# Kernel optimization log

Hardware: AMD Instinct MI355X
Metric: run time of the kernel (lower is better)

The kernel has to match this reference:

```python
import jax, jax.numpy as jnp
import numpy as np

MEM = 256
K = 4
SQRT_MK = 32  # sqrt(MEM*K)
HID = 1024
INP = 1024
B = 8192
EPS = 1e-12


def _linear_params(key, out_f, in_f):
    kw, kb = jax.random.split(key)
    bound = 1.0 / np.sqrt(in_f)
    W = jax.random.uniform(kw, (out_f, in_f), jnp.float32, -bound, bound)
    b = jax.random.uniform(kb, (out_f,), jnp.float32, -bound, bound)
    return W, b


def setup_inputs() -> dict:
    key = jax.random.key(0)
    ks = jax.random.split(key, 8)
    x = jax.random.normal(ks[0], (B, INP), jnp.float32)
    h0 = jax.random.normal(ks[1], (B, HID), jnp.float32)
    memory = jax.random.normal(ks[2], (B, MEM), jnp.float32)
    W_h, b_h = _linear_params(ks[3], HID, MEM + HID + INP)        # hmi2h
    W_a, b_a = _linear_params(ks[4], K, MEM + HID)                # hm2alpha
    W_b, b_b = _linear_params(ks[5], K, MEM + HID)                # hm2beta
    W_va, b_va = _linear_params(ks[6], 2 * SQRT_MK, MEM + HID)    # hm2v_alpha
    W_vb, b_vb = _linear_params(ks[7], 2 * SQRT_MK, MEM + HID)    # hm2v_beta
    return {"x": x, "h0": h0, "memory": memory,
            "W_h": W_h, "b_h": b_h, "W_a": W_a, "b_a": b_a,
            "W_b": W_b, "b_b": b_b, "W_va": W_va, "b_va": b_va,
            "W_vb": W_vb, "b_vb": b_vb}


def _p5_normalize(v):
    # F.normalize(p=5, dim=2): v / max(||v||_5, eps)
    n = jnp.sum(jnp.abs(v) ** 5, axis=2, keepdims=True) ** (1.0 / 5.0)
    return v / jnp.maximum(n, EPS)


def _rank1_v(hm, W, b):
    u = hm @ W.T + b                       # [B, 2*sqrt_mk]
    u0, u1 = u[:, :SQRT_MK], u[:, SQRT_MK:]
    v = (u0[:, :, None] * u1[:, None, :]).reshape(-1, K, MEM)  # outer product
    return _p5_normalize(v)


def reference(x, h0, memory, W_h, b_h, W_a, b_a, W_b, b_b, W_va, b_va, W_vb, b_vb):
    # use_relu=False -> _opt_relu is identity; layer_norm=False -> identity
    c_input = jnp.concatenate([x, h0, memory], axis=1)          # [B, INP+HID+MEM]
    h = jax.nn.relu(c_input @ W_h.T + b_h)                      # [B, HID]
    hm = jnp.concatenate([h, memory], axis=1)                   # [B, HID+MEM]
    alpha = hm @ W_a.T + b_a                                    # [B, K]
    beta = hm @ W_b.T + b_b                                     # [B, K]
    v_alpha = _rank1_v(hm, W_va, b_va)                          # [B, K, MEM]
    v_beta = _rank1_v(hm, W_vb, b_vb)                           # [B, K, MEM]
    delta = alpha[:, :, None] * v_alpha - beta[:, :, None] * v_beta
    memory_new = memory + jnp.mean(delta, axis=1)               # [B, MEM]
    return memory_new, h
```

## Files before the change

### kernel.cpp

```cpp
#include <hip/hip_runtime.h>
#include <stdint.h>

#define B_ROWS 8192
#define INP    1024
#define HID    1024
#define MEMD   256
#define KIN    2304
#define KHM    1280
#define NCAT   144

typedef unsigned short u16;
typedef unsigned int   u32;
typedef __attribute__((ext_vector_type(8))) short bf16x8;
typedef __attribute__((ext_vector_type(4))) float f32x4;

__device__ __forceinline__ u16 f2bf(float f) {
  u32 b = __builtin_bit_cast(u32, f);
  u32 r = b + 0x7FFF + ((b >> 16) & 1);
  return (u16)(r >> 16);
}

__device__ __forceinline__ void gload16(const void* g, void* l) {
  __builtin_amdgcn_global_load_lds(
      (const __attribute__((address_space(1))) u32*)g,
      (__attribute__((address_space(3))) u32*)l, 16, 0, 0);
}

__global__ void k_cvt_xh(const float* __restrict__ x, const float* __restrict__ h0,
                         u16* __restrict__ Abig) {
  const int nIter = B_ROWS * 2048 / 8;
  for (int i = blockIdx.x * blockDim.x + threadIdx.x; i < nIter;
       i += gridDim.x * blockDim.x) {
    int row = i >> 8;
    int col = (i & 255) * 8;
    const float* src = (col < 1024) ? (x + (size_t)row * 1024 + col)
                                    : (h0 + (size_t)row * 1024 + (col - 1024));
    float4 v0 = ((const float4*)src)[0];
    float4 v1 = ((const float4*)src)[1];
    union { u16 u[8]; uint4 q; } pk;
    pk.u[0]=f2bf(v0.x); pk.u[1]=f2bf(v0.y); pk.u[2]=f2bf(v0.z); pk.u[3]=f2bf(v0.w);
    pk.u[4]=f2bf(v1.x); pk.u[5]=f2bf(v1.y); pk.u[6]=f2bf(v1.z); pk.u[7]=f2bf(v1.w);
    *((uint4*)(Abig + (size_t)row * KIN + col)) = pk.q;
  }
}

__global__ void k_cvt_mem(const float* __restrict__ mem,
                          u16* __restrict__ Abig, u16* __restrict__ hm) {
  int i = blockIdx.x * blockDim.x + threadIdx.x;
  int row = i >> 5;
  int col = (i & 31) * 8;
  const float* src = mem + (size_t)row * MEMD + col;
  float4 v0 = ((const float4*)src)[0];
  float4 v1 = ((const float4*)src)[1];
  union { u16 u[8]; uint4 q; } pk;
  pk.u[0]=f2bf(v0.x); pk.u[1]=f2bf(v0.y); pk.u[2]=f2bf(v0.z); pk.u[3]=f2bf(v0.w);
  pk.u[4]=f2bf(v1.x); pk.u[5]=f2bf(v1.y); pk.u[6]=f2bf(v1.z); pk.u[7]=f2bf(v1.w);
  *((uint4*)(Abig + (size_t)row * KIN + 2048 + col)) = pk.q;
  *((uint4*)(hm   + (size_t)row * KHM + 1024 + col)) = pk.q;
}

__global__ void k_cvt_wh(const float* __restrict__ Wh, u16* __restrict__ WhB) {
  int i = blockIdx.x * blockDim.x + threadIdx.x;
  const float* src = Wh + (size_t)i * 8;
  float4 v0 = ((const float4*)src)[0];
  float4 v1 = ((const float4*)src)[1];
  union { u16 u[8]; uint4 q; } pk;
  pk.u[0]=f2bf(v0.x); pk.u[1]=f2bf(v0.y); pk.u[2]=f2bf(v0.z); pk.u[3]=f2bf(v0.w);
  pk.u[4]=f2bf(v1.x); pk.u[5]=f2bf(v1.y); pk.u[6]=f2bf(v1.z); pk.u[7]=f2bf(v1.w);
  *((uint4*)(WhB + (size_t)i * 8)) = pk.q;
}

__global__ void k_cvt_wcat(const float* __restrict__ Wa, const float* __restrict__ ba,
                           const float* __restrict__ Wb, const float* __restrict__ bb,
                           const float* __restrict__ Wva, const float* __restrict__ bva,
                           const float* __restrict__ Wvb, const float* __restrict__ bvb,
                           u16* __restrict__ Wcat, float* __restrict__ bcat) {
  int r = blockIdx.x;
  int t = threadIdx.x;
  const float* src = nullptr; float bias = 0.f;
  if      (r < 4)   { src = Wa  + (size_t)r        * KHM; bias = ba[r];      }
  else if (r < 8)   { src = Wb  + (size_t)(r - 4)  * KHM; bias = bb[r - 4];  }
  else if (r < 72)  { src = Wva + (size_t)(r - 8)  * KHM; bias = bva[r - 8]; }
  else if (r < 136) { src = Wvb + (size_t)(r - 72) * KHM; bias = bvb[r - 72];}
  if (t == 0) bcat[r] = bias;
  if (t < 160) {
    int col = t * 8;
    union { u16 u[8]; uint4 q; } pk;
    if (src) {
      float4 v0 = ((const float4*)(src + col))[0];
      float4 v1 = ((const float4*)(src + col))[1];
      pk.u[0]=f2bf(v0.x); pk.u[1]=f2bf(v0.y); pk.u[2]=f2bf(v0.z); pk.u[3]=f2bf(v0.w);
      pk.u[4]=f2bf(v1.x); pk.u[5]=f2bf(v1.y); pk.u[6]=f2bf(v1.z); pk.u[7]=f2bf(v1.w);
    } else {
      pk.q = make_uint4(0, 0, 0, 0);
    }
    *((uint4*)(Wcat + (size_t)r * KHM + col)) = pk.q;
  }
}

__global__ void __launch_bounds__(256, 2)
k_gemm1(const u16* __restrict__ Abig, const u16* __restrict__ WhB,
        const float* __restrict__ bh,
        float* __restrict__ outH, u16* __restrict__ hm) {
  __shared__ u16 As[2][128 * 64];
  __shared__ u16 Bs[2][128 * 64];
  const int tid = threadIdx.x;
  const int bid = blockIdx.x;
  const int swz = (bid & 7) * 64 + (bid >> 3);
  const int br = swz >> 3;
  const int bc = swz & 7;
  const int wid = tid >> 6, lane = tid & 63;
  const int wr = wid >> 1, wc = wid & 1;
  const int lr = lane & 15, lko = lane >> 4;

  const f32x4 vz = {0.f, 0.f, 0.f, 0.f};
  f32x4 acc[4][4];
#pragma unroll
  for (int m = 0; m < 4; ++m)
#pragma unroll
    for (int n = 0; n < 4; ++n) acc[m][n] = vz;

  const int sRow   = tid >> 3;
  const int sSlotG = (tid & 7) ^ (sRow & 7);
  const u16* gA = Abig + (size_t)(br * 128 + sRow) * KIN + sSlotG * 8;
  const u16* gB = WhB  + (size_t)(bc * 128 + sRow) * KIN + sSlotG * 8;

  const int sx  = lr & 7;
  const int s0  = ((0 + lko) ^ sx) * 8;
  const int s1  = ((4 + lko) ^ sx) * 8;
  const int axr = (wr * 64 + lr) * 64;
  const int bxr = (wc * 64 + lr) * 64;

#pragma unroll
  for (int q = 0; q < 4; ++q) {
    gload16(gA + (size_t)(q * 32) * KIN, &As[0][q * 2048 + tid * 8]);
    gload16(gB + (size_t)(q * 32) * KIN, &Bs[0][q * 2048 + tid * 8]);
  }

  for (int kt = 0; kt < KIN / 64; ++kt) {
    const int cur = kt & 1;
    if (kt < KIN / 64 - 1) {
      const int kofs = (kt + 1) * 64;
#pragma unroll
      for (int q = 0; q < 4; ++q) {
        gload16(gA + (size_t)(q * 32) * KIN + kofs, &As[1 - cur][q * 2048 + tid * 8]);
        gload16(gB + (size_t)(q * 32) * KIN + kofs, &Bs[1 - cur][q * 2048 + tid * 8]);
      }
      asm volatile("s_waitcnt vmcnt(8)" ::: "memory");
    } else {
      asm volatile("s_waitcnt vmcnt(0)" ::: "memory");
    }
    __builtin_amdgcn_s_barrier();
    __builtin_amdgcn_sched_barrier(0);

    const u16* Ac = &As[cur][0];
    const u16* Bc = &Bs[cur][0];
    {
      bf16x8 a[4], b[4];
#pragma unroll
      for (int m = 0; m < 4; ++m) a[m] = *(const bf16x8*)&Ac[axr + m * 1024 + s0];
#pragma unroll
      for (int n = 0; n < 4; ++n) b[n] = *(const bf16x8*)&Bc[bxr + n * 1024 + s0];
      __builtin_amdgcn_s_setprio(1);
#pragma unroll
      for (int m = 0; m < 4; ++m)
#pragma unroll
        for (int n = 0; n < 4; ++n)
          acc[m][n] = __builtin_amdgcn_mfma_f32_16x16x32_bf16(a[m], b[n], acc[m][n], 0, 0, 0);
      __builtin_amdgcn_s_setprio(0);
    }
    {
      bf16x8 a[4], b[4];
#pragma unroll
      for (int m = 0; m < 4; ++m) a[m] = *(const bf16x8*)&Ac[axr + m * 1024 + s1];
#pragma unroll
      for (int n = 0; n < 4; ++n) b[n] = *(const bf16x8*)&Bc[bxr + n * 1024 + s1];
      __builtin_amdgcn_s_setprio(1);
#pragma unroll
      for (int m = 0; m < 4; ++m)
#pragma unroll
        for (int n = 0; n < 4; ++n)
          acc[m][n] = __builtin_amdgcn_mfma_f32_16x16x32_bf16(a[m], b[n], acc[m][n], 0, 0, 0);
      __builtin_amdgcn_s_setprio(0);
    }
    __builtin_amdgcn_sched_barrier(0);
    __builtin_amdgcn_s_barrier();
  }

  const int rowBase = br * 128 + wr * 64;
  const int colBase = bc * 128 + wc * 64;
#pragma unroll
  for (int n = 0; n < 4; ++n) {
    const int col = colBase + n * 16 + lr;
    const float bias = bh[col];
#pragma unroll
    for (int m = 0; m < 4; ++m) {
#pragma unroll
      for (int r = 0; r < 4; ++r) {
        const int row = rowBase + m * 16 + lko * 4 + r;
        float v = fmaxf(acc[m][n][r] + bias, 0.0f);
        outH[(size_t)row * HID + col] = v;
        hm[(size_t)row * KHM + col] = f2bf(v);
      }
    }
  }
}

__device__ __forceinline__ float p5(float x) {
  float a = fabsf(x);
  float a2 = a * a;
  return a2 * a2 * a;
}

__global__ void __launch_bounds__(256, 2)
k_gemm2(const u16* __restrict__ hm, const u16* __restrict__ Wcat,
        const float* __restrict__ bcat,
        const float* __restrict__ mem, float* __restrict__ outM) {
  __shared__ float pS[4][16][148];
  const int tid = threadIdx.x;
  const int bid = blockIdx.x;
  const int wid = tid >> 6, lane = tid & 63;
  const int lr = lane & 15, lko = lane >> 4;
  const int rowBase = bid * 16;

  const f32x4 vz = {0.f, 0.f, 0.f, 0.f};
  f32x4 acc[9];
#pragma unroll
  for (int n = 0; n < 9; ++n) acc[n] = vz;

  const u16* gA = hm   + (size_t)(rowBase + lr) * KHM + lko * 8;
  const u16* gB = Wcat + (size_t)lr * KHM + lko * 8;

  for (int c = 0; c < 5; ++c) {
    const int kofs = (c * 4 + wid) * 64;
#pragma unroll
    for (int h = 0; h < 2; ++h) {
      const int ko = kofs + h * 32;
      bf16x8 a = *(const bf16x8*)(gA + ko);
      bf16x8 b[9];
#pragma unroll
      for (int n = 0; n < 9; ++n)
        b[n] = *(const bf16x8*)(gB + (size_t)(n * 16) * KHM + ko);
#pragma unroll
      for (int n = 0; n < 9; ++n)
        acc[n] = __builtin_amdgcn_mfma_f32_16x16x32_bf16(a, b[n], acc[n], 0, 0, 0);
    }
  }

#pragma unroll
  for (int n = 0; n < 9; ++n)
#pragma unroll
    for (int r = 0; r < 4; ++r)
      pS[wid][lko * 4 + r][n * 16 + lr] = acc[n][r];
  __syncthreads();

  {
    const int rr = tid >> 4;
    const int cb = (tid & 15) * 9;
#pragma unroll
    for (int i = 0; i < 9; ++i) {
      const int col = cb + i;
      float s = pS[0][rr][col] + pS[1][rr][col] + pS[2][rr][col] + pS[3][rr][col]
              + bcat[col];
      pS[0][rr][col] = s;
    }
  }
  __syncthreads();

  const int r = tid >> 4;
  const int t = tid & 15;
  const float* U = &pS[0][r][0];

  float S1a = 0.f, S1b = 0.f;
  {
    const float4* Ua = (const float4*)(U + 40);
    const float4* Ub = (const float4*)(U + 104);
#pragma unroll
    for (int i = 0; i < 8; ++i) {
      float4 va = Ua[i], vb = Ub[i];
      S1a += p5(va.x) + p5(va.y) + p5(va.z) + p5(va.w);
      S1b += p5(vb.x) + p5(vb.y) + p5(vb.z) + p5(vb.w);
    }
  }

  float sa[4], sb[4];
#pragma unroll
  for (int k = 0; k < 4; ++k) {
    const float4* Pa = (const float4*)(U + 8 + 8 * k);
    const float4* Pb = (const float4*)(U + 72 + 8 * k);
    float4 a0v = Pa[0], a1v = Pa[1], b0v = Pb[0], b1v = Pb[1];
    float S0a = p5(a0v.x) + p5(a0v.y) + p5(a0v.z) + p5(a0v.w)
              + p5(a1v.x) + p5(a1v.y) + p5(a1v.z) + p5(a1v.w);
    float S0b = p5(b0v.x) + p5(b0v.y) + p5(b0v.z) + p5(b0v.w)
              + p5(b1v.x) + p5(b1v.y) + p5(b1v.z) + p5(b1v.w);
    float na = exp2f(0.2f * log2f(S0a * S1a));
    float nb = exp2f(0.2f * log2f(S0b * S1b));
    sa[k] = 0.25f * U[k]     / fmaxf(na, 1e-12f);
    sb[k] = 0.25f * U[4 + k] / fmaxf(nb, 1e-12f);
  }

  const int j0 = t >> 1;
  float A0 = 0.f, B0 = 0.f;
#pragma unroll
  for (int k = 0; k < 4; ++k) {
    A0 += sa[k] * U[8  + 8 * k + j0];
    B0 += sb[k] * U[72 + 8 * k + j0];
  }

  const int i1b = (t & 1) * 16;
  const size_t rowg = (size_t)(rowBase + r);
  const float4* memR = (const float4*)(mem  + rowg * MEMD + t * 16);
  float4*       outR = (float4*)      (outM + rowg * MEMD + t * 16);
#pragma unroll
  for (int j = 0; j < 4; ++j) {
    float4 mv = memR[j];
    float4 ua = *(const float4*)(U + 40  + i1b + j * 4);
    float4 ub = *(const float4*)(U + 104 + i1b + j * 4);
    float4 o;
    o.x = mv.x + A0 * ua.x - B0 * ub.x;
    o.y = mv.y + A0 * ua.y - B0 * ub.y;
    o.z = mv.z + A0 * ua.z - B0 * ub.z;
    o.w = mv.w + A0 * ua.w - B0 * ub.w;
    outR[j] = o;
  }
}

extern "C" void kernel_launch(void* const* d_in, const int* in_sizes, int n_in,
                              void* d_out, int out_size, void* d_ws, size_t ws_size,
                              hipStream_t stream) {
  const float* x   = (const float*)d_in[0];
  const float* h0  = (const float*)d_in[1];
  const float* mem = (const float*)d_in[2];
  const float* Wh  = (const float*)d_in[3];
  const float* bh  = (const float*)d_in[4];
  const float* Wa  = (const float*)d_in[5];
  const float* ba  = (const float*)d_in[6];
  const float* Wb  = (const float*)d_in[7];
  const float* bb  = (const float*)d_in[8];
  const float* Wva = (const float*)d_in[9];
  const float* bva = (const float*)d_in[10];
  const float* Wvb = (const float*)d_in[11];
  const float* bvb = (const float*)d_in[12];

  float* outM = (float*)d_out;
  float* outH = (float*)d_out + (size_t)B_ROWS * MEMD;

  char* ws = (char*)d_ws;
  u16*   Abig = (u16*)(ws);
  u16*   WhB  = (u16*)(ws + 37748736);
  u16*   hmB  = (u16*)(ws + 42467328);
  u16*   Wcat = (u16*)(ws + 63438848);
  float* bcat = (float*)(ws + 63807488);

  k_cvt_xh  <<<dim3(2048), dim3(256), 0, stream>>>(x, h0, Abig);
  k_cvt_mem <<<dim3(1024), dim3(256), 0, stream>>>(mem, Abig, hmB);
  k_cvt_wh  <<<dim3(1152), dim3(256), 0, stream>>>(Wh, WhB);
  k_cvt_wcat<<<dim3(144),  dim3(256), 0, stream>>>(Wa, ba, Wb, bb, Wva, bva, Wvb, bvb, Wcat, bcat);
  k_gemm1   <<<dim3(512),  dim3(256), 0, stream>>>(Abig, WhB, bh, outH, hmB);
  k_gemm2   <<<dim3(512),  dim3(256), 0, stream>>>(hmB, Wcat, bcat, mem, outM);
}
```

Baseline: 226.4 us.

## Fuse activation bf16 conversion into GEMM loads and drop staging buffers

Removes the separate x/h0/memory bf16 conversion kernels and the bf16 Abig/hm staging buffers. GEMM1 now loads fp32 activations into registers, converts them, and writes the swizzled bf16 tile to LDS inside its double-buffered loop. GEMM2 reads the fp32 h output and memory directly and converts them in registers. The two weight conversion kernels are merged into one launch. This saves a large round trip through global memory and several launches, but adds VALU conversion work and register pressure inside the GEMM main loop, and GEMM1 re-reads fp32 A tiles, twice the bytes of bf16, for each column block.

```diff
diff --git a/kernel.cpp b/kernel.cpp
--- a/kernel.cpp
+++ b/kernel.cpp
@@ -14,10 +14,13 @@
 typedef __attribute__((ext_vector_type(8))) short bf16x8;
 typedef __attribute__((ext_vector_type(4))) float f32x4;
 
-__device__ __forceinline__ u16 f2bf(float f) {
+__device__ __forceinline__ u32 f2bf_u32(float f) {
   u32 b = __builtin_bit_cast(u32, f);
   u32 r = b + 0x7FFF + ((b >> 16) & 1);
-  return (u16)(r >> 16);
+  return r >> 16;
+}
+__device__ __forceinline__ u32 pk2(float lo, float hi) {
+  return f2bf_u32(lo) | (f2bf_u32(hi) << 16);
 }
 
 __device__ __forceinline__ void gload16(const void* g, void* l) {
@@ -26,82 +29,51 @@
       (__attribute__((address_space(3))) u32*)l, 16, 0, 0);
 }
 
-__global__ void k_cvt_xh(const float* __restrict__ x, const float* __restrict__ h0,
-                         u16* __restrict__ Abig) {
-  const int nIter = B_ROWS * 2048 / 8;
-  for (int i = blockIdx.x * blockDim.x + threadIdx.x; i < nIter;
-       i += gridDim.x * blockDim.x) {
-    int row = i >> 8;
-    int col = (i & 255) * 8;
-    const float* src = (col < 1024) ? (x + (size_t)row * 1024 + col)
-                                    : (h0 + (size_t)row * 1024 + (col - 1024));
+__global__ void k_cvt_w(const float* __restrict__ Wh,
+                        const float* __restrict__ Wa, const float* __restrict__ ba,
+                        const float* __restrict__ Wb, const float* __restrict__ bb,
+                        const float* __restrict__ Wva, const float* __restrict__ bva,
+                        const float* __restrict__ Wvb, const float* __restrict__ bvb,
+                        u16* __restrict__ WhB, u16* __restrict__ Wcat,
+                        float* __restrict__ bcat) {
+  const int blk = blockIdx.x;
+  if (blk < 1152) {
+    const int i = blk * 256 + threadIdx.x;
+    const float* src = Wh + (size_t)i * 8;
     float4 v0 = ((const float4*)src)[0];
     float4 v1 = ((const float4*)src)[1];
-    union { u16 u[8]; uint4 q; } pk;
-    pk.u[0]=f2bf(v0.x); pk.u[1]=f2bf(v0.y); pk.u[2]=f2bf(v0.z); pk.u[3]=f2bf(v0.w);
-    pk.u[4]=f2bf(v1.x); pk.u[5]=f2bf(v1.y); pk.u[6]=f2bf(v1.z); pk.u[7]=f2bf(v1.w);
-    *((uint4*)(Abig + (size_t)row * KIN + col)) = pk.q;
-  }
-}
-
-__global__ void k_cvt_mem(const float* __restrict__ mem,
-                          u16* __restrict__ Abig, u16* __restrict__ hm) {
-  int i = blockIdx.x * blockDim.x + threadIdx.x;
-  int row = i >> 5;
-  int col = (i & 31) * 8;
-  const float* src = mem + (size_t)row * MEMD + col;
-  float4 v0 = ((const float4*)src)[0];
-  float4 v1 = ((const float4*)src)[1];
-  union { u16 u[8]; uint4 q; } pk;
-  pk.u[0]=f2bf(v0.x); pk.u[1]=f2bf(v0.y); pk.u[2]=f2bf(v0.z); pk.u[3]=f2bf(v0.w);
-  pk.u[4]=f2bf(v1.x); pk.u[5]=f2bf(v1.y); pk.u[6]=f2bf(v1.z); pk.u[7]=f2bf(v1.w);
-  *((uint4*)(Abig + (size_t)row * KIN + 2048 + col)) = pk.q;
-  *((uint4*)(hm   + (size_t)row * KHM + 1024 + col)) = pk.q;
-}
-
-__global__ void k_cvt_wh(const float* __restrict__ Wh, u16* __restrict__ WhB) {
-  int i = blockIdx.x * blockDim.x + threadIdx.x;
-  const float* src = Wh + (size_t)i * 8;
-  float4 v0 = ((const float4*)src)[0];
-  float4 v1 = ((const float4*)src)[1];
-  union { u16 u[8]; uint4 q; } pk;
-  pk.u[0]=f2bf(v0.x); pk.u[1]=f2bf(v0.y); pk.u[2]=f2bf(v0.z); pk.u[3]=f2bf(v0.w);
-  pk.u[4]=f2bf(v1.x); pk.u[5]=f2bf(v1.y); pk.u[6]=f2bf(v1.z); pk.u[7]=f2bf(v1.w);
-  *((uint4*)(WhB + (size_t)i * 8)) = pk.q;
-}
-
-__global__ void k_cvt_wcat(const float* __restrict__ Wa, const float* __restrict__ ba,
-                           const float* __restrict__ Wb, const float* __restrict__ bb,
-                           const float* __restrict__ Wva, const float* __restrict__ bva,
-                           const float* __restrict__ Wvb, const float* __restrict__ bvb,
-                           u16* __restrict__ Wcat, float* __restrict__ bcat) {
-  int r = blockIdx.x;
-  int t = threadIdx.x;
-  const float* src = nullptr; float bias = 0.f;
-  if      (r < 4)   { src = Wa  + (size_t)r        * KHM; bias = ba[r];      }
-  else if (r < 8)   { src = Wb  + (size_t)(r - 4)  * KHM; bias = bb[r - 4];  }
-  else if (r < 72)  { src = Wva + (size_t)(r - 8)  * KHM; bias = bva[r - 8]; }
-  else if (r < 136) { src = Wvb + (size_t)(r - 72) * KHM; bias = bvb[r - 72];}
-  if (t == 0) bcat[r] = bias;
-  if (t < 160) {
-    int col = t * 8;
-    union { u16 u[8]; uint4 q; } pk;
-    if (src) {
-      float4 v0 = ((const float4*)(src + col))[0];
-      float4 v1 = ((const float4*)(src + col))[1];
-      pk.u[0]=f2bf(v0.x); pk.u[1]=f2bf(v0.y); pk.u[2]=f2bf(v0.z); pk.u[3]=f2bf(v0.w);
-      pk.u[4]=f2bf(v1.x); pk.u[5]=f2bf(v1.y); pk.u[6]=f2bf(v1.z); pk.u[7]=f2bf(v1.w);
-    } else {
-      pk.q = make_uint4(0, 0, 0, 0);
-    }
-    *((uint4*)(Wcat + (size_t)r * KHM + col)) = pk.q;
+    uint4 q = make_uint4(pk2(v0.x, v0.y), pk2(v0.z, v0.w),
+                         pk2(v1.x, v1.y), pk2(v1.z, v1.w));
+    *((uint4*)(WhB + (size_t)i * 8)) = q;
+  } else {
+    const int r = blk - 1152;
+    const int t = threadIdx.x;
+    const float* src = nullptr; float bias = 0.f;
+    if      (r < 4)   { src = Wa  + (size_t)r        * KHM; bias = ba[r];      }
+    else if (r < 8)   { src = Wb  + (size_t)(r - 4)  * KHM; bias = bb[r - 4];  }
+    else if (r < 72)  { src = Wva + (size_t)(r - 8)  * KHM; bias = bva[r - 8]; }
+    else if (r < 136) { src = Wvb + (size_t)(r - 72) * KHM; bias = bvb[r - 72];}
+    if (t == 0) bcat[r] = bias;
+    if (t < 160) {
+      const int col = t * 8;
+      uint4 q;
+      if (src) {
+        float4 v0 = ((const float4*)(src + col))[0];
+        float4 v1 = ((const float4*)(src + col))[1];
+        q = make_uint4(pk2(v0.x, v0.y), pk2(v0.z, v0.w),
+                       pk2(v1.x, v1.y), pk2(v1.z, v1.w));
+      } else {
+        q = make_uint4(0, 0, 0, 0);
+      }
+      *((uint4*)(Wcat + (size_t)r * KHM + col)) = q;
+    }
   }
 }
 
 __global__ void __launch_bounds__(256, 2)
-k_gemm1(const u16* __restrict__ Abig, const u16* __restrict__ WhB,
-        const float* __restrict__ bh,
-        float* __restrict__ outH, u16* __restrict__ hm) {
+k_gemm1(const float* __restrict__ x, const float* __restrict__ h0,
+        const float* __restrict__ mem, const u16* __restrict__ WhB,
+        const float* __restrict__ bh, float* __restrict__ outH) {
   __shared__ u16 As[2][128 * 64];
   __shared__ u16 Bs[2][128 * 64];
   const int tid = threadIdx.x;
@@ -121,9 +93,10 @@
     for (int n = 0; n < 4; ++n) acc[m][n] = vz;
 
   const int sRow   = tid >> 3;
-  const int sSlotG = (tid & 7) ^ (sRow & 7);
-  const u16* gA = Abig + (size_t)(br * 128 + sRow) * KIN + sSlotG * 8;
-  const u16* gB = WhB  + (size_t)(bc * 128 + sRow) * KIN + sSlotG * 8;
+  const int sCol8  = tid & 7;
+  const int dSlot  = sCol8 ^ (sRow & 7);
+  const int sSlotG = sCol8 ^ (sRow & 7);
+  const u16* gB = WhB + (size_t)(bc * 128 + sRow) * KIN + sSlotG * 8;
 
   const int sx  = lr & 7;
   const int s0  = ((0 + lko) ^ sx) * 8;
@@ -131,24 +104,52 @@
   const int axr = (wr * 64 + lr) * 64;
   const int bxr = (wc * 64 + lr) * 64;
 
-#pragma unroll
-  for (int q = 0; q < 4; ++q) {
-    gload16(gA + (size_t)(q * 32) * KIN, &As[0][q * 2048 + tid * 8]);
-    gload16(gB + (size_t)(q * 32) * KIN, &Bs[0][q * 2048 + tid * 8]);
-  }
-
-  for (int kt = 0; kt < KIN / 64; ++kt) {
-    const int cur = kt & 1;
-    if (kt < KIN / 64 - 1) {
+  auto srcBase = [&](int kt) -> const float* {
+    if (kt < 16) return x   + (size_t)(br * 128 + sRow) * 1024 + kt * 64 + sCol8 * 8;
+    if (kt < 32) return h0  + (size_t)(br * 128 + sRow) * 1024 + (kt - 16) * 64 + sCol8 * 8;
+    return            mem + (size_t)(br * 128 + sRow) * 256  + (kt - 32) * 64 + sCol8 * 8;
+  };
+  auto srcStride = [&](int kt) -> int { return (kt < 32) ? 1024 : 256; };
+
+  float4 pre[4][2];
+
+  {
+    const float* p = srcBase(0);
+    const int st = srcStride(0);
+#pragma unroll
+    for (int q = 0; q < 4; ++q) {
+      pre[q][0] = ((const float4*)(p + (size_t)(q * 32) * st))[0];
+      pre[q][1] = ((const float4*)(p + (size_t)(q * 32) * st))[1];
+    }
+#pragma unroll
+    for (int q = 0; q < 4; ++q)
+      gload16(gB + (size_t)(q * 32) * KIN, &Bs[0][q * 2048 + tid * 8]);
+#pragma unroll
+    for (int q = 0; q < 4; ++q) {
+      uint4 pk = make_uint4(pk2(pre[q][0].x, pre[q][0].y), pk2(pre[q][0].z, pre[q][0].w),
+                            pk2(pre[q][1].x, pre[q][1].y), pk2(pre[q][1].z, pre[q][1].w));
+      *((uint4*)&As[0][(q * 32 + sRow) * 64 + dSlot * 8]) = pk;
+    }
+  }
+
+  const int NKT = KIN / 64;
+  for (int kt = 0; kt < NKT; ++kt) {
+    const int cur = kt & 1, nxt = 1 - cur;
+    if (kt < NKT - 1) {
+      const float* p = srcBase(kt + 1);
+      const int st = srcStride(kt + 1);
+#pragma unroll
+      for (int q = 0; q < 4; ++q) {
+        pre[q][0] = ((const float4*)(p + (size_t)(q * 32) * st))[0];
+        pre[q][1] = ((const float4*)(p + (size_t)(q * 32) * st))[1];
+      }
       const int kofs = (kt + 1) * 64;
 #pragma unroll
-      for (int q = 0; q < 4; ++q) {
-        gload16(gA + (size_t)(q * 32) * KIN + kofs, &As[1 - cur][q * 2048 + tid * 8]);
-        gload16(gB + (size_t)(q * 32) * KIN + kofs, &Bs[1 - cur][q * 2048 + tid * 8]);
-      }
-      asm volatile("s_waitcnt vmcnt(8)" ::: "memory");
+      for (int q = 0; q < 4; ++q)
+        gload16(gB + (size_t)(q * 32) * KIN + kofs, &Bs[nxt][q * 2048 + tid * 8]);
+      asm volatile("s_waitcnt vmcnt(12) lgkmcnt(0)" ::: "memory");
     } else {
-      asm volatile("s_waitcnt vmcnt(0)" ::: "memory");
+      asm volatile("s_waitcnt vmcnt(0) lgkmcnt(0)" ::: "memory");
     }
     __builtin_amdgcn_s_barrier();
     __builtin_amdgcn_sched_barrier(0);
@@ -184,6 +185,17 @@
       __builtin_amdgcn_s_setprio(0);
     }
     __builtin_amdgcn_sched_barrier(0);
+
+    if (kt < NKT - 1) {
+      asm volatile("s_waitcnt vmcnt(4)" ::: "memory");
+#pragma unroll
+      for (int q = 0; q < 4; ++q) {
+        uint4 pk = make_uint4(pk2(pre[q][0].x, pre[q][0].y), pk2(pre[q][0].z, pre[q][0].w),
+                              pk2(pre[q][1].x, pre[q][1].y), pk2(pre[q][1].z, pre[q][1].w));
+        *((uint4*)&As[nxt][(q * 32 + sRow) * 64 + dSlot * 8]) = pk;
+      }
+      asm volatile("s_waitcnt lgkmcnt(0)" ::: "memory");
+    }
     __builtin_amdgcn_s_barrier();
   }
 
@@ -200,7 +212,6 @@
         const int row = rowBase + m * 16 + lko * 4 + r;
         float v = fmaxf(acc[m][n][r] + bias, 0.0f);
         outH[(size_t)row * HID + col] = v;
-        hm[(size_t)row * KHM + col] = f2bf(v);
       }
     }
   }
@@ -213,9 +224,9 @@
 }
 
 __global__ void __launch_bounds__(256, 2)
-k_gemm2(const u16* __restrict__ hm, const u16* __restrict__ Wcat,
-        const float* __restrict__ bcat,
-        const float* __restrict__ mem, float* __restrict__ outM) {
+k_gemm2(const float* __restrict__ hfull, const float* __restrict__ memf,
+        const u16* __restrict__ Wcat, const float* __restrict__ bcat,
+        float* __restrict__ outM) {
   __shared__ float pS[4][16][148];
   const int tid = threadIdx.x;
   const int bid = blockIdx.x;
@@ -228,22 +239,29 @@
 #pragma unroll
   for (int n = 0; n < 9; ++n) acc[n] = vz;
 
-  const u16* gA = hm   + (size_t)(rowBase + lr) * KHM + lko * 8;
   const u16* gB = Wcat + (size_t)lr * KHM + lko * 8;
 
+#pragma unroll
   for (int c = 0; c < 5; ++c) {
-    const int kofs = (c * 4 + wid) * 64;
+    const int ck = c * 4 + wid;
+    const float* gAf = (ck < 16)
+        ? hfull + (size_t)(rowBase + lr) * 1024 + ck * 64 + lko * 8
+        : memf  + (size_t)(rowBase + lr) * 256  + (ck - 16) * 64 + lko * 8;
 #pragma unroll
     for (int h = 0; h < 2; ++h) {
-      const int ko = kofs + h * 32;
-      bf16x8 a = *(const bf16x8*)(gA + ko);
+      float4 a0 = ((const float4*)(gAf + h * 32))[0];
+      float4 a1 = ((const float4*)(gAf + h * 32))[1];
+      union { u32 w[4]; bf16x8 v; } ap;
+      ap.w[0] = pk2(a0.x, a0.y); ap.w[1] = pk2(a0.z, a0.w);
+      ap.w[2] = pk2(a1.x, a1.y); ap.w[3] = pk2(a1.z, a1.w);
+      const int ko = ck * 64 + h * 32;
       bf16x8 b[9];
 #pragma unroll
       for (int n = 0; n < 9; ++n)
         b[n] = *(const bf16x8*)(gB + (size_t)(n * 16) * KHM + ko);
 #pragma unroll
       for (int n = 0; n < 9; ++n)
-        acc[n] = __builtin_amdgcn_mfma_f32_16x16x32_bf16(a, b[n], acc[n], 0, 0, 0);
+        acc[n] = __builtin_amdgcn_mfma_f32_16x16x32_bf16(ap.v, b[n], acc[n], 0, 0, 0);
     }
   }
 
@@ -309,7 +327,7 @@
 
   const int i1b = (t & 1) * 16;
   const size_t rowg = (size_t)(rowBase + r);
-  const float4* memR = (const float4*)(mem  + rowg * MEMD + t * 16);
+  const float4* memR = (const float4*)(memf + rowg * MEMD + t * 16);
   float4*       outR = (float4*)      (outM + rowg * MEMD + t * 16);
 #pragma unroll
   for (int j = 0; j < 4; ++j) {
@@ -346,16 +364,13 @@
   float* outH = (float*)d_out + (size_t)B_ROWS * MEMD;
 
   char* ws = (char*)d_ws;
-  u16*   Abig = (u16*)(ws);
-  u16*   WhB  = (u16*)(ws + 37748736);
-  u16*   hmB  = (u16*)(ws + 42467328);
-  u16*   Wcat = (u16*)(ws + 63438848);
-  float* bcat = (float*)(ws + 63807488);
-
-  k_cvt_xh  <<<dim3(2048), dim3(256), 0, stream>>>(x, h0, Abig);
-  k_cvt_mem <<<dim3(1024), dim3(256), 0, stream>>>(mem, Abig, hmB);
-  k_cvt_wh  <<<dim3(1152), dim3(256), 0, stream>>>(Wh, WhB);
-  k_cvt_wcat<<<dim3(144),  dim3(256), 0, stream>>>(Wa, ba, Wb, bb, Wva, bva, Wvb, bvb, Wcat, bcat);
-  k_gemm1   <<<dim3(512),  dim3(256), 0, stream>>>(Abig, WhB, bh, outH, hmB);
-  k_gemm2   <<<dim3(512),  dim3(256), 0, stream>>>(hmB, Wcat, bcat, mem, outM);
-}
+  u16*   WhB  = (u16*)(ws);
+  u16*   Wcat = (u16*)(ws + 4718592);
+  float* bcat = (float*)(ws + 5087232);
+
+  k_cvt_w <<<dim3(1296), dim3(256), 0, stream>>>(Wh, Wa, ba, Wb, bb,
+                                                 Wva, bva, Wvb, bvb,
+                                                 WhB, Wcat, bcat);
+  k_gemm1 <<<dim3(512),  dim3(256), 0, stream>>>(x, h0, mem, WhB, bh, outH);
+  k_gemm2 <<<dim3(512),  dim3(256), 0, stream>>>(outH, mem, Wcat, bcat, outM);
+}
```

New measurement: 243.3 us. 1.07x slower.
